# Optimization experiments

Measured on AMD Instinct MI355X. Metric: run time of the kernel, lower is better.

Reference implementation:

```python
import jax, jax.numpy as jnp
import numpy as np

B, T, F, H = 2048, 512, 32, 128  # batch, seq_len, input_features, hidden_units

def _xavier(key, shape):
    fan_in, fan_out = shape[1], shape[0]
    limit = float(np.sqrt(6.0 / (fan_in + fan_out)))
    return jax.random.uniform(key, shape, jnp.float32, -limit, limit)

def setup_inputs() -> dict:
    key = jax.random.key(0)
    ks = jax.random.split(key, 8)
    x = jax.random.normal(ks[0], (B, T, F), jnp.float32)
    # PyTorch LSTM weights: weight_ih_l{k} [4H, in], weight_hh_l{k} [4H, H]; biases init to zeros.
    Wih0 = _xavier(ks[1], (4 * H, F))
    Whh0 = _xavier(ks[2], (4 * H, H))
    b0 = jnp.zeros((4 * H,), jnp.float32)  # b_ih + b_hh (both zero-init)
    Wih1 = _xavier(ks[3], (4 * H, H))
    Whh1 = _xavier(ks[4], (4 * H, H))
    b1 = jnp.zeros((4 * H,), jnp.float32)
    Wfc = _xavier(ks[5], (1, H))
    bfc = jnp.zeros((1,), jnp.float32)
    return dict(x=x, Wih0=Wih0, Whh0=Whh0, b0=b0, Wih1=Wih1, Whh1=Whh1, b1=b1, Wfc=Wfc, bfc=bfc)

def _lstm_layer(x, Wih, Whh, b):
    # x: [B, T, Din] -> outputs h over time: [B, T, H]
    pre = jnp.einsum('btf,gf->btg', x, Wih) + b  # precompute input projections [B, T, 4H]
    h0 = jnp.zeros((x.shape[0], Whh.shape[1]), x.dtype)

    def step(carry, p_t):
        h, c = carry
        z = p_t + h @ Whh.T  # [B, 4H]
        i, f, g, o = jnp.split(z, 4, axis=-1)  # PyTorch gate order: i, f, g, o
        i = jax.nn.sigmoid(i)
        f = jax.nn.sigmoid(f)
        g = jnp.tanh(g)
        o = jax.nn.sigmoid(o)
        c = f * c + i * g
        h = o * jnp.tanh(c)
        return (h, c), h

    (_, _), hs = jax.lax.scan(step, (h0, h0), jnp.swapaxes(pre, 0, 1))  # hs: [T, B, H]
    return jnp.swapaxes(hs, 0, 1)

def reference(x, Wih0, Whh0, b0, Wih1, Whh1, b1, Wfc, bfc):
    h = _lstm_layer(x, Wih0, Whh0, b0)   # layer 0 (dropout off in eval)
    h = _lstm_layer(h, Wih1, Whh1, b1)   # layer 1
    last = h[:, -1, :]                   # [B, H]
    return last @ Wfc.T + bfc            # [B, 1]
```

## Files before the change

### kernel.cpp

```cpp
#include <hip/hip_runtime.h>
#include <stdint.h>


#define B_ 2048
#define T_ 512
#define F_ 32
#define H_ 128
#define LSTR 144
#define H0SZ (8 * LSTR)
#define W1STR 8192

#define LOG2E 1.4426950408889634f

typedef _Float16 half8 __attribute__((ext_vector_type(8)));
typedef float float4_t __attribute__((ext_vector_type(4)));

#define BARRIER_LGKM() asm volatile("s_waitcnt lgkmcnt(0)\n\ts_barrier" ::: "memory")

__device__ __forceinline__ float fexp2(float x) {
  float r; asm("v_exp_f32 %0, %1" : "=v"(r) : "v"(x)); return r;
}
__device__ __forceinline__ float frcp(float x) { return __builtin_amdgcn_rcpf(x); }

__device__ __forceinline__ half8 cvt2f4(float4_t a, float4_t b) {
  half8 r;
  r[0] = (_Float16)a[0]; r[1] = (_Float16)a[1]; r[2] = (_Float16)a[2]; r[3] = (_Float16)a[3];
  r[4] = (_Float16)b[0]; r[5] = (_Float16)b[1]; r[6] = (_Float16)b[2]; r[7] = (_Float16)b[3];
  return r;
}
__device__ __forceinline__ half8 load8cvt(const float* p) {
  return cvt2f4(*(const float4_t*)p, *(const float4_t*)(p + 4));
}

__global__ __launch_bounds__(512, 2) void lstm_fused(
    const float* __restrict__ x, const float* __restrict__ Wih0,
    const float* __restrict__ Whh0, const float* __restrict__ b0,
    const float* __restrict__ Wih1, const float* __restrict__ Whh1,
    const float* __restrict__ b1, const float* __restrict__ Wfc,
    const float* __restrict__ bfc, float* __restrict__ out)
{
  __shared__ __attribute__((aligned(16))) _Float16 lds_w1[8 * W1STR];
  __shared__ __attribute__((aligned(16))) _Float16 lds_h0[2 * H0SZ];
  __shared__ __attribute__((aligned(16))) _Float16 lds_h1[2 * H0SZ];
  __shared__ float lds_fc[8][8];

  const int tid  = threadIdx.x;
  const int w    = tid >> 6;
  const int lane = tid & 63;
  const int n    = lane & 15;
  const int q    = lane >> 4;
  const int rbase = (int)blockIdx.x * 8;
  const int rload = rbase + (n & 7);
  const int rsh  = (q >> 1) * 2;
  const int rowq = (q & 1) * 4;
  const int colg = w * 16 + n;
  const int aoff = (n & 7) * LSTR + q * 8;

  half8 bwih0[4], bwhh0[4][4], bwhh1[4][4];
  _Float16* w1base = lds_w1 + w * W1STR + q * 128 + n * 8;
#pragma unroll
  for (int j = 0; j < 4; ++j) {
    const int g = j * H_ + colg;
    bwih0[j] = load8cvt(Wih0 + g * F_ + q * 8);
#pragma unroll
    for (int kc = 0; kc < 4; ++kc) {
      bwhh0[j][kc] = load8cvt(Whh0 + g * H_ + kc * 32 + q * 8);
      bwhh1[j][kc] = load8cvt(Whh1 + g * H_ + kc * 32 + q * 8);
      *(half8*)(w1base + (kc * 4 + j) * 512) = load8cvt(Wih1 + g * H_ + kc * 32 + q * 8);
    }
  }
  const float cI0 = -b0[0 * H_ + colg] * LOG2E;
  const float cF0 = -b0[1 * H_ + colg] * LOG2E;
  const float cG0 =  b0[2 * H_ + colg] * (2.0f * LOG2E);
  const float cO0 = -b0[3 * H_ + colg] * LOG2E;
  const float cI1 = -b1[0 * H_ + colg] * LOG2E;
  const float cF1 = -b1[1 * H_ + colg] * LOG2E;
  const float cG1 =  b1[2 * H_ + colg] * (2.0f * LOG2E);
  const float cO1 = -b1[3 * H_ + colg] * LOG2E;

  for (int i = tid; i < 2 * H0SZ; i += 512) { lds_h0[i] = (_Float16)0.0f; lds_h1[i] = (_Float16)0.0f; }
  __syncthreads();

  const float4_t zC = {0.f, 0.f, 0.f, 0.f};
  float c00 = 0.f, c01 = 0.f;
  float c10 = 0.f, c11 = 0.f;

  const float* xptr = x + rload * (T_ * F_) + q * 8;
  float4_t xrA = *(const float4_t*)(xptr);
  float4_t xrB = *(const float4_t*)(xptr + 4);

#pragma unroll 1
  for (int tau = 0; tau <= T_; ++tau) {
    const int pw = tau & 1;
    _Float16* h0rd = lds_h0 + (pw ^ 1) * H0SZ;
    _Float16* h0wr = lds_h0 + pw * H0SZ;
    _Float16* h1rd = lds_h1 + pw * H0SZ;
    _Float16* h1wr = lds_h1 + (pw ^ 1) * H0SZ;
    const bool do0 = (tau < T_), do1 = (tau >= 1);

    half8 ah[4];
#pragma unroll
    for (int kc = 0; kc < 4; ++kc)
      ah[kc] = *(const half8*)(h0rd + aoff + kc * 32);
    half8 w1a[4];
#pragma unroll
    for (int j = 0; j < 4; ++j)
      w1a[j] = *(const half8*)(w1base + (0 * 4 + j) * 512);

    float4_t acc0[4];
    if (do0) {
      half8 ax = cvt2f4(xrA, xrB);
#pragma unroll
      for (int j = 0; j < 4; ++j)
        acc0[j] = __builtin_amdgcn_mfma_f32_16x16x32_f16(ax, bwih0[j], zC, 0, 0, 0);
#pragma unroll
      for (int kc = 0; kc < 4; ++kc)
#pragma unroll
        for (int j = 0; j < 4; ++j)
          acc0[j] = __builtin_amdgcn_mfma_f32_16x16x32_f16(ah[kc], bwhh0[j][kc], acc0[j], 0, 0, 0);
      const int tn = (tau + 1 < T_) ? tau + 1 : T_ - 1;
      xrA = *(const float4_t*)(xptr + tn * F_);
      xrB = *(const float4_t*)(xptr + tn * F_ + 4);
    }
    if (do0) {
#pragma unroll
      for (int rr = 0; rr < 2; ++rr) {
        const int ri = rsh + rr;
        const float gi = frcp(1.0f + fexp2(__builtin_fmaf(acc0[0][ri], -LOG2E, cI0)));
        const float gf = frcp(1.0f + fexp2(__builtin_fmaf(acc0[1][ri], -LOG2E, cF0)));
        const float gg = 1.0f - 2.0f * frcp(1.0f + fexp2(__builtin_fmaf(acc0[2][ri], 2.0f * LOG2E, cG0)));
        const float go = frcp(1.0f + fexp2(__builtin_fmaf(acc0[3][ri], -LOG2E, cO0)));
        float& cc = rr ? c01 : c00;
        cc = __builtin_fmaf(gf, cc, gi * gg);
        const float th = 1.0f - 2.0f * frcp(1.0f + fexp2(cc * (2.0f * LOG2E)));
        h0wr[(rowq + ri) * LSTR + colg] = (_Float16)(go * th);
      }
    }
    if (do1) {
      float4_t acc1[4];
      half8 w1b[4];
#pragma unroll
      for (int j = 0; j < 4; ++j)
        w1b[j] = *(const half8*)(w1base + (1 * 4 + j) * 512);
#pragma unroll
      for (int j = 0; j < 4; ++j)
        acc1[j] = __builtin_amdgcn_mfma_f32_16x16x32_f16(ah[0], w1a[j], zC, 0, 0, 0);
#pragma unroll
      for (int j = 0; j < 4; ++j)
        w1a[j] = *(const half8*)(w1base + (2 * 4 + j) * 512);
#pragma unroll
      for (int j = 0; j < 4; ++j)
        acc1[j] = __builtin_amdgcn_mfma_f32_16x16x32_f16(ah[1], w1b[j], acc1[j], 0, 0, 0);
#pragma unroll
      for (int j = 0; j < 4; ++j)
        w1b[j] = *(const half8*)(w1base + (3 * 4 + j) * 512);
#pragma unroll
      for (int j = 0; j < 4; ++j)
        acc1[j] = __builtin_amdgcn_mfma_f32_16x16x32_f16(ah[2], w1a[j], acc1[j], 0, 0, 0);
      half8 a1h[4];
#pragma unroll
      for (int kc = 0; kc < 4; ++kc)
        a1h[kc] = *(const half8*)(h1rd + aoff + kc * 32);
#pragma unroll
      for (int j = 0; j < 4; ++j)
        acc1[j] = __builtin_amdgcn_mfma_f32_16x16x32_f16(ah[3], w1b[j], acc1[j], 0, 0, 0);
#pragma unroll
      for (int kc = 0; kc < 4; ++kc)
#pragma unroll
        for (int j = 0; j < 4; ++j)
          acc1[j] = __builtin_amdgcn_mfma_f32_16x16x32_f16(a1h[kc], bwhh1[j][kc], acc1[j], 0, 0, 0);
#pragma unroll
      for (int rr = 0; rr < 2; ++rr) {
        const int ri = rsh + rr;
        const float gi = frcp(1.0f + fexp2(__builtin_fmaf(acc1[0][ri], -LOG2E, cI1)));
        const float gf = frcp(1.0f + fexp2(__builtin_fmaf(acc1[1][ri], -LOG2E, cF1)));
        const float gg = 1.0f - 2.0f * frcp(1.0f + fexp2(__builtin_fmaf(acc1[2][ri], 2.0f * LOG2E, cG1)));
        const float go = frcp(1.0f + fexp2(__builtin_fmaf(acc1[3][ri], -LOG2E, cO1)));
        float& cc = rr ? c11 : c10;
        cc = __builtin_fmaf(gf, cc, gi * gg);
        const float th = 1.0f - 2.0f * frcp(1.0f + fexp2(cc * (2.0f * LOG2E)));
        h1wr[(rowq + ri) * LSTR + colg] = (_Float16)(go * th);
      }
    }
    BARRIER_LGKM();
  }

  const float wfcv = Wfc[colg];
  float p0 = (float)lds_h1[H0SZ + (rowq + rsh + 0) * LSTR + colg] * wfcv;
  float p1 = (float)lds_h1[H0SZ + (rowq + rsh + 1) * LSTR + colg] * wfcv;
#pragma unroll
  for (int m = 1; m < 16; m <<= 1) {
    p0 += __shfl_xor(p0, m);
    p1 += __shfl_xor(p1, m);
  }
  if (n == 0) {
    lds_fc[w][rowq + rsh + 0] = p0;
    lds_fc[w][rowq + rsh + 1] = p1;
  }
  __syncthreads();
  if (tid < 8) {
    float s = bfc[0];
#pragma unroll
    for (int wv = 0; wv < 8; ++wv) s += lds_fc[wv][tid];
    out[rbase + tid] = s;
  }
}

extern "C" void kernel_launch(void* const* d_in, const int* in_sizes, int n_in,
                              void* d_out, int out_size, void* d_ws, size_t ws_size,
                              hipStream_t stream) {
  const float* x    = (const float*)d_in[0];
  const float* Wih0 = (const float*)d_in[1];
  const float* Whh0 = (const float*)d_in[2];
  const float* b0   = (const float*)d_in[3];
  const float* Wih1 = (const float*)d_in[4];
  const float* Whh1 = (const float*)d_in[5];
  const float* b1   = (const float*)d_in[6];
  const float* Wfc  = (const float*)d_in[7];
  const float* bfc  = (const float*)d_in[8];
  float* outp = (float*)d_out;
  (void)d_ws; (void)ws_size;

  lstm_fused<<<B_ / 8, 512, 0, stream>>>(x, Wih0, Whh0, b0, Wih1, Whh1, b1,
                                         Wfc, bfc, outp);
}
```

Measured before the change: 980.4 us.

## Peel first and last timesteps and interleave layer-0 gates with layer-1 MFMAs

Peels the first iteration (layer 0 only) and the last (layer 1 only) out of the wavefront loop, so the steady-state body has no do0/do1 branches. Inside the body, the layer-1 input-projection MFMAs are issued before the layer-0 gate math, and the h1 LDS reads come after it. This lets transcendental VALU work overlap the MFMA pipeline and hides LDS latency. The cost is larger code and more live registers, which could hurt occupancy at 2 blocks per CU.

```diff
diff --git a/kernel.cpp b/kernel.cpp
--- a/kernel.cpp
+++ b/kernel.cpp
@@ -89,14 +89,41 @@
   float4_t xrA = *(const float4_t*)(xptr);
   float4_t xrB = *(const float4_t*)(xptr + 4);
 
+  auto GATES = [&](float4_t (&acc)[4], float cI, float cF, float cG, float cO,
+                   float& ca, float& cb, _Float16* dst) {
+#pragma unroll
+    for (int rr = 0; rr < 2; ++rr) {
+      const int ri = rsh + rr;
+      const float gi = frcp(1.0f + fexp2(__builtin_fmaf(acc[0][ri], -LOG2E, cI)));
+      const float gf = frcp(1.0f + fexp2(__builtin_fmaf(acc[1][ri], -LOG2E, cF)));
+      const float gg = 1.0f - 2.0f * frcp(1.0f + fexp2(__builtin_fmaf(acc[2][ri], 2.0f * LOG2E, cG)));
+      const float go = frcp(1.0f + fexp2(__builtin_fmaf(acc[3][ri], -LOG2E, cO)));
+      float& cc = rr ? cb : ca;
+      cc = __builtin_fmaf(gf, cc, gi * gg);
+      const float th = 1.0f - 2.0f * frcp(1.0f + fexp2(cc * (2.0f * LOG2E)));
+      dst[(rowq + ri) * LSTR + colg] = (_Float16)(go * th);
+    }
+  };
+
+  {
+    float4_t acc0[4];
+    half8 ax = cvt2f4(xrA, xrB);
+#pragma unroll
+    for (int j = 0; j < 4; ++j)
+      acc0[j] = __builtin_amdgcn_mfma_f32_16x16x32_f16(ax, bwih0[j], zC, 0, 0, 0);
+    xrA = *(const float4_t*)(xptr + F_);
+    xrB = *(const float4_t*)(xptr + F_ + 4);
+    GATES(acc0, cI0, cF0, cG0, cO0, c00, c01, lds_h0 );
+    BARRIER_LGKM();
+  }
+
 #pragma unroll 1
-  for (int tau = 0; tau <= T_; ++tau) {
+  for (int tau = 1; tau < T_; ++tau) {
     const int pw = tau & 1;
     _Float16* h0rd = lds_h0 + (pw ^ 1) * H0SZ;
     _Float16* h0wr = lds_h0 + pw * H0SZ;
     _Float16* h1rd = lds_h1 + pw * H0SZ;
     _Float16* h1wr = lds_h1 + (pw ^ 1) * H0SZ;
-    const bool do0 = (tau < T_), do1 = (tau >= 1);
 
     half8 ah[4];
 #pragma unroll
@@ -108,81 +135,105 @@
       w1a[j] = *(const half8*)(w1base + (0 * 4 + j) * 512);
 
     float4_t acc0[4];
-    if (do0) {
-      half8 ax = cvt2f4(xrA, xrB);
+    half8 ax = cvt2f4(xrA, xrB);
+#pragma unroll
+    for (int j = 0; j < 4; ++j)
+      acc0[j] = __builtin_amdgcn_mfma_f32_16x16x32_f16(ax, bwih0[j], zC, 0, 0, 0);
+#pragma unroll
+    for (int kc = 0; kc < 4; ++kc)
 #pragma unroll
       for (int j = 0; j < 4; ++j)
-        acc0[j] = __builtin_amdgcn_mfma_f32_16x16x32_f16(ax, bwih0[j], zC, 0, 0, 0);
-#pragma unroll
-      for (int kc = 0; kc < 4; ++kc)
-#pragma unroll
-        for (int j = 0; j < 4; ++j)
-          acc0[j] = __builtin_amdgcn_mfma_f32_16x16x32_f16(ah[kc], bwhh0[j][kc], acc0[j], 0, 0, 0);
-      const int tn = (tau + 1 < T_) ? tau + 1 : T_ - 1;
-      xrA = *(const float4_t*)(xptr + tn * F_);
-      xrB = *(const float4_t*)(xptr + tn * F_ + 4);
-    }
-    if (do0) {
-#pragma unroll
-      for (int rr = 0; rr < 2; ++rr) {
-        const int ri = rsh + rr;
-        const float gi = frcp(1.0f + fexp2(__builtin_fmaf(acc0[0][ri], -LOG2E, cI0)));
-        const float gf = frcp(1.0f + fexp2(__builtin_fmaf(acc0[1][ri], -LOG2E, cF0)));
-        const float gg = 1.0f - 2.0f * frcp(1.0f + fexp2(__builtin_fmaf(acc0[2][ri], 2.0f * LOG2E, cG0)));
-        const float go = frcp(1.0f + fexp2(__builtin_fmaf(acc0[3][ri], -LOG2E, cO0)));
-        float& cc = rr ? c01 : c00;
-        cc = __builtin_fmaf(gf, cc, gi * gg);
-        const float th = 1.0f - 2.0f * frcp(1.0f + fexp2(cc * (2.0f * LOG2E)));
-        h0wr[(rowq + ri) * LSTR + colg] = (_Float16)(go * th);
-      }
-    }
-    if (do1) {
-      float4_t acc1[4];
-      half8 w1b[4];
+        acc0[j] = __builtin_amdgcn_mfma_f32_16x16x32_f16(ah[kc], bwhh0[j][kc], acc0[j], 0, 0, 0);
+    const int tn = (tau + 1 < T_) ? tau + 1 : T_ - 1;
+    xrA = *(const float4_t*)(xptr + tn * F_);
+    xrB = *(const float4_t*)(xptr + tn * F_ + 4);
+
+    float4_t acc1[4];
+    half8 w1b[4];
+#pragma unroll
+    for (int j = 0; j < 4; ++j)
+      w1b[j] = *(const half8*)(w1base + (1 * 4 + j) * 512);
+#pragma unroll
+    for (int j = 0; j < 4; ++j)
+      acc1[j] = __builtin_amdgcn_mfma_f32_16x16x32_f16(ah[0], w1a[j], zC, 0, 0, 0);
+#pragma unroll
+    for (int j = 0; j < 4; ++j)
+      w1a[j] = *(const half8*)(w1base + (2 * 4 + j) * 512);
+#pragma unroll
+    for (int j = 0; j < 4; ++j)
+      acc1[j] = __builtin_amdgcn_mfma_f32_16x16x32_f16(ah[1], w1b[j], acc1[j], 0, 0, 0);
+#pragma unroll
+    for (int j = 0; j < 4; ++j)
+      w1b[j] = *(const half8*)(w1base + (3 * 4 + j) * 512);
+#pragma unroll
+    for (int j = 0; j < 4; ++j)
+      acc1[j] = __builtin_amdgcn_mfma_f32_16x16x32_f16(ah[2], w1a[j], acc1[j], 0, 0, 0);
+#pragma unroll
+    for (int j = 0; j < 4; ++j)
+      acc1[j] = __builtin_amdgcn_mfma_f32_16x16x32_f16(ah[3], w1b[j], acc1[j], 0, 0, 0);
+
+    GATES(acc0, cI0, cF0, cG0, cO0, c00, c01, h0wr);
+
+    half8 a1h[4];
+#pragma unroll
+    for (int kc = 0; kc < 4; ++kc)
+      a1h[kc] = *(const half8*)(h1rd + aoff + kc * 32);
+#pragma unroll
+    for (int kc = 0; kc < 4; ++kc)
 #pragma unroll
       for (int j = 0; j < 4; ++j)
-        w1b[j] = *(const half8*)(w1base + (1 * 4 + j) * 512);
+        acc1[j] = __builtin_amdgcn_mfma_f32_16x16x32_f16(a1h[kc], bwhh1[j][kc], acc1[j], 0, 0, 0);
+
+    GATES(acc1, cI1, cF1, cG1, cO1, c10, c11, h1wr);
+    BARRIER_LGKM();
+  }
+
+  {
+    _Float16* h0rd = lds_h0 + H0SZ;
+    _Float16* h1rd = lds_h1;
+    _Float16* h1wr = lds_h1 + H0SZ;
+
+    half8 ah[4];
+#pragma unroll
+    for (int kc = 0; kc < 4; ++kc)
+      ah[kc] = *(const half8*)(h0rd + aoff + kc * 32);
+    float4_t acc1[4];
+    half8 w1a[4], w1b[4];
+#pragma unroll
+    for (int j = 0; j < 4; ++j)
+      w1a[j] = *(const half8*)(w1base + (0 * 4 + j) * 512);
+#pragma unroll
+    for (int j = 0; j < 4; ++j)
+      w1b[j] = *(const half8*)(w1base + (1 * 4 + j) * 512);
+#pragma unroll
+    for (int j = 0; j < 4; ++j)
+      acc1[j] = __builtin_amdgcn_mfma_f32_16x16x32_f16(ah[0], w1a[j], zC, 0, 0, 0);
+#pragma unroll
+    for (int j = 0; j < 4; ++j)
+      w1a[j] = *(const half8*)(w1base + (2 * 4 + j) * 512);
+#pragma unroll
+    for (int j = 0; j < 4; ++j)
+      acc1[j] = __builtin_amdgcn_mfma_f32_16x16x32_f16(ah[1], w1b[j], acc1[j], 0, 0, 0);
+#pragma unroll
+    for (int j = 0; j < 4; ++j)
+      w1b[j] = *(const half8*)(w1base + (3 * 4 + j) * 512);
+#pragma unroll
+    for (int j = 0; j < 4; ++j)
+      acc1[j] = __builtin_amdgcn_mfma_f32_16x16x32_f16(ah[2], w1a[j], acc1[j], 0, 0, 0);
+#pragma unroll
+    for (int j = 0; j < 4; ++j)
+      acc1[j] = __builtin_amdgcn_mfma_f32_16x16x32_f16(ah[3], w1b[j], acc1[j], 0, 0, 0);
+    half8 a1h[4];
+#pragma unroll
+    for (int kc = 0; kc < 4; ++kc)
+      a1h[kc] = *(const half8*)(h1rd + aoff + kc * 32);
+#pragma unroll
+    for (int kc = 0; kc < 4; ++kc)
 #pragma unroll
       for (int j = 0; j < 4; ++j)
-        acc1[j] = __builtin_amdgcn_mfma_f32_16x16x32_f16(ah[0], w1a[j], zC, 0, 0, 0);
-#pragma unroll
-      for (int j = 0; j < 4; ++j)
-        w1a[j] = *(const half8*)(w1base + (2 * 4 + j) * 512);
-#pragma unroll
-      for (int j = 0; j < 4; ++j)
-        acc1[j] = __builtin_amdgcn_mfma_f32_16x16x32_f16(ah[1], w1b[j], acc1[j], 0, 0, 0);
-#pragma unroll
-      for (int j = 0; j < 4; ++j)
-        w1b[j] = *(const half8*)(w1base + (3 * 4 + j) * 512);
-#pragma unroll
-      for (int j = 0; j < 4; ++j)
-        acc1[j] = __builtin_amdgcn_mfma_f32_16x16x32_f16(ah[2], w1a[j], acc1[j], 0, 0, 0);
-      half8 a1h[4];
-#pragma unroll
-      for (int kc = 0; kc < 4; ++kc)
-        a1h[kc] = *(const half8*)(h1rd + aoff + kc * 32);
-#pragma unroll
-      for (int j = 0; j < 4; ++j)
-        acc1[j] = __builtin_amdgcn_mfma_f32_16x16x32_f16(ah[3], w1b[j], acc1[j], 0, 0, 0);
-#pragma unroll
-      for (int kc = 0; kc < 4; ++kc)
-#pragma unroll
-        for (int j = 0; j < 4; ++j)
-          acc1[j] = __builtin_amdgcn_mfma_f32_16x16x32_f16(a1h[kc], bwhh1[j][kc], acc1[j], 0, 0, 0);
-#pragma unroll
-      for (int rr = 0; rr < 2; ++rr) {
-        const int ri = rsh + rr;
-        const float gi = frcp(1.0f + fexp2(__builtin_fmaf(acc1[0][ri], -LOG2E, cI1)));
-        const float gf = frcp(1.0f + fexp2(__builtin_fmaf(acc1[1][ri], -LOG2E, cF1)));
-        const float gg = 1.0f - 2.0f * frcp(1.0f + fexp2(__builtin_fmaf(acc1[2][ri], 2.0f * LOG2E, cG1)));
-        const float go = frcp(1.0f + fexp2(__builtin_fmaf(acc1[3][ri], -LOG2E, cO1)));
-        float& cc = rr ? c11 : c10;
-        cc = __builtin_fmaf(gf, cc, gi * gg);
-        const float th = 1.0f - 2.0f * frcp(1.0f + fexp2(cc * (2.0f * LOG2E)));
-        h1wr[(rowq + ri) * LSTR + colg] = (_Float16)(go * th);
-      }
-    }
-    BARRIER_LGKM();
+        acc1[j] = __builtin_amdgcn_mfma_f32_16x16x32_f16(a1h[kc], bwhh1[j][kc], acc1[j], 0, 0, 0);
+    GATES(acc1, cI1, cF1, cG1, cO1, c10, c11, h1wr);
+    asm volatile("s_waitcnt lgkmcnt(0)" ::: "memory");
   }
 
   const float wfcv = Wfc[colg];
```

New measurement: 998.1 us. Within noise of the previous version (+1.8%).
